# Performance work log

Measured on AMD Instinct MI355X. Metric: run time of the kernel, lower is better.

The kernel has to match this reference:

```python
import jax, jax.numpy as jnp
import numpy as np

D_MODEL = 1024
NUM_HEADS = 16
HEAD_DIM = D_MODEL // NUM_HEADS  # 64
# NOTE: the torch module passes scale=attention_head_size (NOT 1/sqrt(dh));
# we reproduce that exact math: scores are MULTIPLIED by head_dim.
SCALE = float(HEAD_DIM)

B, S = 2, 2048


def setup_inputs() -> dict:
    key = jax.random.key(0)
    ks = jax.random.split(key, 6)
    q = jax.random.normal(ks[0], (B, S, D_MODEL), dtype=jnp.float32)
    k = jax.random.normal(ks[1], (B, S, D_MODEL), dtype=jnp.float32)
    v = jax.random.normal(ks[2], (B, S, D_MODEL), dtype=jnp.float32)
    # Linear weights stored as [in, out]; scaled like typical init so the
    # (head_dim-scaled) logits stay numerically sane.
    w_std = 0.02
    Wq = jax.random.normal(ks[3], (D_MODEL, D_MODEL), dtype=jnp.float32) * w_std
    Wk = jax.random.normal(ks[4], (D_MODEL, D_MODEL), dtype=jnp.float32) * w_std
    Wv = jax.random.normal(ks[5], (D_MODEL, D_MODEL), dtype=jnp.float32) * w_std
    return {"q": q, "k": k, "v": v, "Wq": Wq, "Wk": Wk, "Wv": Wv}


def reference(q, k, v, Wq, Wk, Wv):
    Bq, Sq, _ = q.shape
    # QKV projections (qkv_bias=False), split into heads: [B, S, H, dh]
    qh = (q @ Wq).reshape(Bq, Sq, NUM_HEADS, HEAD_DIM)
    kh = (k @ Wk).reshape(Bq, Sq, NUM_HEADS, HEAD_DIM)
    vh = (v @ Wv).reshape(Bq, Sq, NUM_HEADS, HEAD_DIM)
    # Full materialized scores [B, H, Sq, Sk] -- the naive MHA pattern.
    sims = jnp.einsum("bqhd,bkhd->bhqk", qh, kh) * SCALE
    attn = jax.nn.softmax(sims, axis=-1)
    # Second matmul, then merge heads back: [B, S, D]
    out = jnp.einsum("bhqk,bkhd->bqhd", attn, vh).reshape(Bq, Sq, D_MODEL)
    return out
```

## Files before the change

### kernel.cpp

```cpp
#include <hip/hip_runtime.h>
#include <cstdint>
#include <cstddef>

typedef unsigned short u16;
typedef __bf16 bf16x8 __attribute__((ext_vector_type(8)));
typedef float f32x4 __attribute__((ext_vector_type(4)));
typedef unsigned int u32x4 __attribute__((ext_vector_type(4)));
typedef u16 u16x4 __attribute__((ext_vector_type(4)));

typedef __attribute__((address_space(3))) void lds_void;
typedef __attribute__((address_space(1))) void glb_void;

constexpr size_t XSZ = 4096ull * 1024ull;
constexpr size_t WSZ = 1024ull * 1024ull;
constexpr size_t OFF_XQH = 0;
constexpr size_t OFF_XQL = OFF_XQH + XSZ;
constexpr size_t OFF_XKH = OFF_XQL + XSZ;
constexpr size_t OFF_XKL = OFF_XKH + XSZ;
constexpr size_t OFF_XVH = OFF_XKL + XSZ;
constexpr size_t OFF_XVL = OFF_XVH + XSZ;
constexpr size_t OFF_WQH = OFF_XVL + XSZ;
constexpr size_t OFF_WQL = OFF_WQH + WSZ;
constexpr size_t OFF_WKH = OFF_WQL + WSZ;
constexpr size_t OFF_WKL = OFF_WKH + WSZ;
constexpr size_t OFF_WVH = OFF_WKL + WSZ;
constexpr size_t OFF_WVL = OFF_WVH + WSZ;
constexpr size_t OFF_QH  = OFF_WVL + WSZ;
constexpr size_t OFF_QL  = OFF_QH + XSZ;
constexpr size_t OFF_KH  = OFF_QL + XSZ;
constexpr size_t OFF_KL  = OFF_KH + XSZ;
constexpr size_t OFF_VH  = OFF_KL + XSZ;
constexpr size_t OFF_VT  = OFF_VH + XSZ;

__device__ __forceinline__ u16 f2b(float f) {
  unsigned u = __builtin_bit_cast(unsigned, f);
  return (u16)((u + 0x7FFFu + ((u >> 16) & 1u)) >> 16);
}
__device__ __forceinline__ float b2f(u16 h) {
  return __builtin_bit_cast(float, ((unsigned)h) << 16);
}
__device__ __forceinline__ bf16x8 ld8(const u16* p) {
  return __builtin_bit_cast(bf16x8, *(const u32x4*)p);
}
__device__ __forceinline__ unsigned pk2(float a, float b) {
#if __has_builtin(__builtin_amdgcn_cvt_pk_bf16_f32)
  auto v = __builtin_amdgcn_cvt_pk_bf16_f32(a, b);
  return __builtin_bit_cast(unsigned, v);
#else
  return (unsigned)f2b(a) | ((unsigned)f2b(b) << 16);
#endif
}
__device__ __forceinline__ void glds16(const u16* g, u16* l) {
  __builtin_amdgcn_global_load_lds((const glb_void*)g, (lds_void*)l, 16, 0, 0);
}
__device__ __forceinline__ int swz32(int row, int cg) {
  return row * 32 + ((cg ^ ((row >> 1) & 3)) * 8);
}
__device__ __forceinline__ int swz64(int row, int cg) {
  return row * 64 + ((cg ^ (row & 7)) * 8);
}

__global__ __launch_bounds__(256) void convert_x3(const float* __restrict__ q,
                                                  const float* __restrict__ k,
                                                  const float* __restrict__ v,
                                                  u16* __restrict__ ws) {
  int z = blockIdx.y;
  const float* in = (z == 0) ? q : (z == 1) ? k : v;
  u16* hi = ws + ((z == 0) ? OFF_XQH : (z == 1) ? OFF_XKH : OFF_XVH);
  u16* lo = ws + ((z == 0) ? OFF_XQL : (z == 1) ? OFF_XKL : OFF_XVL);
  size_t i = ((size_t)blockIdx.x * 256u + threadIdx.x) * 4u;
  float4 vv = *(const float4*)(in + i);
  float a[4] = {vv.x, vv.y, vv.z, vv.w};
  u16x4 hv, lv;
#pragma unroll
  for (int j = 0; j < 4; ++j) {
    u16 hb = f2b(a[j]);
    hv[j] = hb;
    lv[j] = f2b(a[j] - b2f(hb));
  }
  *(u16x4*)(hi + i) = hv;
  *(u16x4*)(lo + i) = lv;
}

__global__ __launch_bounds__(256) void convert_w3(const float* __restrict__ Wq,
                                                  const float* __restrict__ Wk,
                                                  const float* __restrict__ Wv,
                                                  u16* __restrict__ ws) {
  int z = blockIdx.z;
  const float* W = (z == 0) ? Wq : (z == 1) ? Wk : Wv;
  u16* hiT = ws + ((z == 0) ? OFF_WQH : (z == 1) ? OFF_WKH : OFF_WVH);
  u16* loT = ws + ((z == 0) ? OFF_WQL : (z == 1) ? OFF_WKL : OFF_WVL);
  __shared__ float tile[32][33];
  int n0 = blockIdx.x * 32, k0 = blockIdx.y * 32;
  int t = threadIdx.x;
  int r = t >> 3, c0 = (t & 7) * 4;
  float4 v = *(const float4*)(W + (size_t)(k0 + r) * 1024 + n0 + c0);
  tile[r][c0] = v.x; tile[r][c0 + 1] = v.y; tile[r][c0 + 2] = v.z; tile[r][c0 + 3] = v.w;
  __syncthreads();
  u16x4 hv, lv;
#pragma unroll
  for (int j = 0; j < 4; ++j) {
    float x = tile[c0 + j][r];
    u16 hb = f2b(x);
    hv[j] = hb;
    lv[j] = f2b(x - b2f(hb));
  }
  size_t o = (size_t)(n0 + r) * 1024 + k0 + c0;
  *(u16x4*)(hiT + o) = hv;
  *(u16x4*)(loT + o) = lv;
}

__global__ __launch_bounds__(256) void gemm_qkv(u16* __restrict__ ws) {
  __shared__ u16 lah[128 * 32];
  __shared__ u16 lal[128 * 32];
  __shared__ u16 lbh[128 * 32];
  __shared__ u16 lbl[128 * 32];
  int z = blockIdx.z;
  const u16 *Ah, *Al, *Bh, *Bl; u16 *Oh, *Ol; bool split;
  if (z == 0)      { Ah = ws + OFF_XQH; Al = ws + OFF_XQL; Bh = ws + OFF_WQH; Bl = ws + OFF_WQL; Oh = ws + OFF_QH; Ol = ws + OFF_QL; split = true; }
  else if (z == 1) { Ah = ws + OFF_XKH; Al = ws + OFF_XKL; Bh = ws + OFF_WKH; Bl = ws + OFF_WKL; Oh = ws + OFF_KH; Ol = ws + OFF_KL; split = true; }
  else             { Ah = ws + OFF_XVH; Al = ws + OFF_XVH; Bh = ws + OFF_WVH; Bl = ws + OFF_WVH; Oh = ws + OFF_VH; Ol = nullptr;    split = false; }
  int m0 = blockIdx.y * 128, n0 = blockIdx.x * 128;
  int t = threadIdx.x, lane = t & 63, wave = t >> 6;
  int wm = (wave >> 1) * 64, wn = (wave & 1) * 64;
  int rl = lane >> 2, cgl = lane & 3;
  f32x4 acc[4][4] = {};
  for (int kb = 0; kb < 32; ++kb) {
    int k0 = kb * 32;
    __syncthreads();
#pragma unroll
    for (int i = 0; i < 2; ++i) {
      int row = wave * 32 + i * 16 + rl;
      int cgg = cgl ^ ((row >> 1) & 3);
      size_t ga = (size_t)(m0 + row) * 1024 + k0 + cgg * 8;
      size_t gb = (size_t)(n0 + row) * 1024 + k0 + cgg * 8;
      int lbase = (wave * 32 + i * 16) * 32;
      glds16(Ah + ga, &lah[lbase]);
      glds16(Bh + gb, &lbh[lbase]);
      if (split) {
        glds16(Al + ga, &lal[lbase]);
        glds16(Bl + gb, &lbl[lbase]);
      }
    }
    __syncthreads();
    int cg0 = lane >> 4;
    bf16x8 afh[4], afl[4], bfh[4], bfl[4];
#pragma unroll
    for (int i = 0; i < 4; ++i) {
      int ra = wm + i * 16 + (lane & 15);
      int rb = wn + i * 16 + (lane & 15);
      afh[i] = ld8(&lah[swz32(ra, cg0)]);
      bfh[i] = ld8(&lbh[swz32(rb, cg0)]);
      if (split) {
        afl[i] = ld8(&lal[swz32(ra, cg0)]);
        bfl[i] = ld8(&lbl[swz32(rb, cg0)]);
      }
    }
#pragma unroll
    for (int mt = 0; mt < 4; ++mt)
#pragma unroll
      for (int nt = 0; nt < 4; ++nt) {
        acc[mt][nt] = __builtin_amdgcn_mfma_f32_16x16x32_bf16(afh[mt], bfh[nt], acc[mt][nt], 0, 0, 0);
        if (split) {
          acc[mt][nt] = __builtin_amdgcn_mfma_f32_16x16x32_bf16(afl[mt], bfh[nt], acc[mt][nt], 0, 0, 0);
          acc[mt][nt] = __builtin_amdgcn_mfma_f32_16x16x32_bf16(afh[mt], bfl[nt], acc[mt][nt], 0, 0, 0);
        }
      }
  }
#pragma unroll
  for (int mt = 0; mt < 4; ++mt)
#pragma unroll
    for (int nt = 0; nt < 4; ++nt)
#pragma unroll
      for (int r = 0; r < 4; ++r) {
        int gm = m0 + wm + mt * 16 + (lane >> 4) * 4 + r;
        int gn = n0 + wn + nt * 16 + (lane & 15);
        int bb = gm >> 11, s = gm & 2047, hh = gn >> 6, d = gn & 63;
        size_t oi = ((size_t)(bb * 16 + hh) * 2048 + s) * 64 + d;
        float val = acc[mt][nt][r];
        u16 hb = f2b(val);
        Oh[oi] = hb;
        if (Ol) Ol[oi] = f2b(val - b2f(hb));
      }
}

__global__ __launch_bounds__(256) void transpose_v(const u16* __restrict__ vh,
                                                   u16* __restrict__ vt) {
  __shared__ u16 tile[64][72];
  int bh = blockIdx.y;
  int s0 = blockIdx.x * 64;
  int t = threadIdx.x;
  for (int c = t; c < 512; c += 256) {
    int row = c >> 3, off = (c & 7) * 8;
    *(u32x4*)(&tile[row][off]) = *(const u32x4*)(vh + ((size_t)bh * 2048 + s0 + row) * 64 + off);
  }
  __syncthreads();
  int d = t >> 2, i0 = (t & 3) * 16;
  u16 vals[16];
#pragma unroll
  for (int i = 0; i < 16; ++i) vals[i] = tile[i0 + i][d];
  u16* outp = vt + ((size_t)bh * 64 + d) * 2048 + s0 + i0;
  *(u32x4*)(outp)     = *(u32x4*)(&vals[0]);
  *(u32x4*)(outp + 8) = *(u32x4*)(&vals[8]);
}

__global__ __launch_bounds__(256) void attn(const u16* __restrict__ ws,
                                            float* __restrict__ out) {
  constexpr int LD = 72;
  constexpr float CEXP = 92.33248261689366f;
  __shared__ u16 lkh[64 * 64];
  __shared__ u16 lkl[64 * 64];
  __shared__ u16 lvt[64 * 64];
  __shared__ u16 lp[4][16 * LD];
  const u16* Qh = ws + OFF_QH; const u16* Ql = ws + OFF_QL;
  const u16* Kh = ws + OFF_KH; const u16* Kl = ws + OFF_KL;
  const u16* Vt = ws + OFF_VT;
  int b = blockIdx.z, h = blockIdx.y;
  int q0 = blockIdx.x * 64;
  int t = threadIdx.x, lane = t & 63, wave = t >> 6;
  size_t hb = (size_t)(b * 16 + h) * (2048 * 64);
  bf16x8 onesf;
#pragma unroll
  for (int j = 0; j < 8; ++j) onesf[j] = __builtin_bit_cast(__bf16, (u16)0x3F80);
  int qrow = q0 + wave * 16 + (lane & 15);
  bf16x8 qfh[2], qfl[2];
#pragma unroll
  for (int ks = 0; ks < 2; ++ks) {
    size_t qo = hb + (size_t)qrow * 64 + ks * 32 + (lane >> 4) * 8;
    qfh[ks] = ld8(Qh + qo);
    qfl[ks] = ld8(Ql + qo);
  }
  float mi[4];
  f32x4 lsum = {};
  f32x4 o[4] = {};
#pragma unroll
  for (int r = 0; r < 4; ++r) mi[r] = -1e30f;
  int rl = lane >> 3, cgl = lane & 7;

  for (int kt = 0; kt < 32; ++kt) {
    __syncthreads();
#pragma unroll
    for (int i = 0; i < 2; ++i) {
      int row = wave * 16 + i * 8 + rl;
      int cgg = cgl ^ (row & 7);
      int lbase = (wave * 16 + i * 8) * 64;
      size_t gk = hb + (size_t)(kt * 64 + row) * 64 + cgg * 8;
      glds16(Kh + gk, &lkh[lbase]);
      glds16(Kl + gk, &lkl[lbase]);
      size_t gv = hb + (size_t)row * 2048 + kt * 64 + cgg * 8;
      glds16(Vt + gv, &lvt[lbase]);
    }
    __syncthreads();
    f32x4 sc[4] = {};
#pragma unroll
    for (int nt = 0; nt < 4; ++nt) {
#pragma unroll
      for (int ks = 0; ks < 2; ++ks) {
        int so = swz64(nt * 16 + (lane & 15), ks * 4 + (lane >> 4));
        bf16x8 bh_ = ld8(&lkh[so]);
        bf16x8 bl_ = ld8(&lkl[so]);
        sc[nt] = __builtin_amdgcn_mfma_f32_16x16x32_bf16(qfh[ks], bh_, sc[nt], 0, 0, 0);
        sc[nt] = __builtin_amdgcn_mfma_f32_16x16x32_bf16(qfl[ks], bh_, sc[nt], 0, 0, 0);
        sc[nt] = __builtin_amdgcn_mfma_f32_16x16x32_bf16(qfh[ks], bl_, sc[nt], 0, 0, 0);
      }
    }
    float mloc[4];
#pragma unroll
    for (int r = 0; r < 4; ++r)
      mloc[r] = fmaxf(fmaxf(sc[0][r], sc[1][r]), fmaxf(sc[2][r], sc[3][r]));
#pragma unroll
    for (int off = 1; off < 16; off <<= 1)
#pragma unroll
      for (int r = 0; r < 4; ++r)
        mloc[r] = fmaxf(mloc[r], __shfl_xor(mloc[r], off));
    float alpha[4], negmc[4];
#pragma unroll
    for (int r = 0; r < 4; ++r) {
      float mn = fmaxf(mi[r], mloc[r]);
      alpha[r] = exp2f((mi[r] - mn) * CEXP);
      mi[r] = mn;
      negmc[r] = -mn * CEXP;
    }
    int q4r = (lane >> 4) * 4;
    u16* lpw = &lp[wave][0];
#pragma unroll
    for (int nt = 0; nt < 4; ++nt) {
      float e0 = exp2f(fmaf(sc[nt][0], CEXP, negmc[0]));
      float e1 = exp2f(fmaf(sc[nt][1], CEXP, negmc[1]));
      float e2 = exp2f(fmaf(sc[nt][2], CEXP, negmc[2]));
      float e3 = exp2f(fmaf(sc[nt][3], CEXP, negmc[3]));
      unsigned u01 = pk2(e0, e1), u23 = pk2(e2, e3);
      int col = nt * 16 + (lane & 15);
      lpw[(q4r + 0) * LD + col] = (u16)(u01 & 0xffffu);
      lpw[(q4r + 1) * LD + col] = (u16)(u01 >> 16);
      lpw[(q4r + 2) * LD + col] = (u16)(u23 & 0xffffu);
      lpw[(q4r + 3) * LD + col] = (u16)(u23 >> 16);
    }
#pragma unroll
    for (int r = 0; r < 4; ++r) {
      lsum[r] *= alpha[r];
      o[0][r] *= alpha[r]; o[1][r] *= alpha[r]; o[2][r] *= alpha[r]; o[3][r] *= alpha[r];
    }
    asm volatile("s_waitcnt lgkmcnt(0)" ::: "memory");
    bf16x8 pa[2];
#pragma unroll
    for (int ks = 0; ks < 2; ++ks)
      pa[ks] = ld8(&lpw[(lane & 15) * LD + ks * 32 + (lane >> 4) * 8]);
    lsum = __builtin_amdgcn_mfma_f32_16x16x32_bf16(pa[0], onesf, lsum, 0, 0, 0);
    lsum = __builtin_amdgcn_mfma_f32_16x16x32_bf16(pa[1], onesf, lsum, 0, 0, 0);
#pragma unroll
    for (int nt = 0; nt < 4; ++nt)
#pragma unroll
      for (int ks = 0; ks < 2; ++ks) {
        bf16x8 bv = ld8(&lvt[swz64(nt * 16 + (lane & 15), ks * 4 + (lane >> 4))]);
        o[nt] = __builtin_amdgcn_mfma_f32_16x16x32_bf16(pa[ks], bv, o[nt], 0, 0, 0);
      }
  }
  float inv[4];
#pragma unroll
  for (int r = 0; r < 4; ++r) inv[r] = 1.0f / lsum[r];
#pragma unroll
  for (int nt = 0; nt < 4; ++nt)
#pragma unroll
    for (int r = 0; r < 4; ++r) {
      int srow = q0 + wave * 16 + (lane >> 4) * 4 + r;
      int d = nt * 16 + (lane & 15);
      out[(size_t)(b * 2048 + srow) * 1024 + h * 64 + d] = o[nt][r] * inv[r];
    }
}

extern "C" void kernel_launch(void* const* d_in, const int* in_sizes, int n_in,
                              void* d_out, int out_size, void* d_ws, size_t ws_size,
                              hipStream_t stream) {
  const float* q  = (const float*)d_in[0];
  const float* k  = (const float*)d_in[1];
  const float* v  = (const float*)d_in[2];
  const float* Wq = (const float*)d_in[3];
  const float* Wk = (const float*)d_in[4];
  const float* Wv = (const float*)d_in[5];
  u16* ws = (u16*)d_ws;
  float* out = (float*)d_out;

  convert_x3<<<dim3(4096, 3), 256, 0, stream>>>(q, k, v, ws);
  convert_w3<<<dim3(32, 32, 3), 256, 0, stream>>>(Wq, Wk, Wv, ws);
  gemm_qkv<<<dim3(8, 32, 3), 256, 0, stream>>>(ws);
  transpose_v<<<dim3(32, 32), 256, 0, stream>>>(ws + OFF_VH, ws + OFF_VT);
  attn<<<dim3(32, 16, 2), 256, 0, stream>>>(ws, out);
}
```

Baseline: 309.2 us.

## Fold softmax scale into Q projection and transpose score MFMA for per-lane row max

Multiplies the Q projection output by the log2-scaled softmax constant inside the QKV GEMM epilogue, so the attention loop can call exp2 directly on scores without a per-element FMA. Swaps the MFMA operand order so each lane holds one query row's scores, reducing the row-max to two cross-lane shuffles and a single running max per lane, with alpha redistributed via shuffles. P tiles are written to LDS as 8-byte vector stores with an XOR swizzle instead of scalar 2-byte stores into a padded layout. Scaling Q before the bf16 hi/lo split changes rounding slightly.

```diff
diff --git a/kernel.cpp b/kernel.cpp
--- a/kernel.cpp
+++ b/kernel.cpp
@@ -6,10 +6,13 @@
 typedef __bf16 bf16x8 __attribute__((ext_vector_type(8)));
 typedef float f32x4 __attribute__((ext_vector_type(4)));
 typedef unsigned int u32x4 __attribute__((ext_vector_type(4)));
+typedef unsigned int u32x2 __attribute__((ext_vector_type(2)));
 typedef u16 u16x4 __attribute__((ext_vector_type(4)));
 
 typedef __attribute__((address_space(3))) void lds_void;
 typedef __attribute__((address_space(1))) void glb_void;
+
+constexpr float CEXP = 92.33248261689366f;
 
 constexpr size_t XSZ = 4096ull * 1024ull;
 constexpr size_t WSZ = 1024ull * 1024ull;
@@ -120,6 +123,7 @@
   if (z == 0)      { Ah = ws + OFF_XQH; Al = ws + OFF_XQL; Bh = ws + OFF_WQH; Bl = ws + OFF_WQL; Oh = ws + OFF_QH; Ol = ws + OFF_QL; split = true; }
   else if (z == 1) { Ah = ws + OFF_XKH; Al = ws + OFF_XKL; Bh = ws + OFF_WKH; Bl = ws + OFF_WKL; Oh = ws + OFF_KH; Ol = ws + OFF_KL; split = true; }
   else             { Ah = ws + OFF_XVH; Al = ws + OFF_XVH; Bh = ws + OFF_WVH; Bl = ws + OFF_WVH; Oh = ws + OFF_VH; Ol = nullptr;    split = false; }
+  float oscale = (z == 0) ? CEXP : 1.0f;
   int m0 = blockIdx.y * 128, n0 = blockIdx.x * 128;
   int t = threadIdx.x, lane = t & 63, wave = t >> 6;
   int wm = (wave >> 1) * 64, wn = (wave & 1) * 64;
@@ -177,7 +181,7 @@
         int gn = n0 + wn + nt * 16 + (lane & 15);
         int bb = gm >> 11, s = gm & 2047, hh = gn >> 6, d = gn & 63;
         size_t oi = ((size_t)(bb * 16 + hh) * 2048 + s) * 64 + d;
-        float val = acc[mt][nt][r];
+        float val = acc[mt][nt][r] * oscale;
         u16 hb = f2b(val);
         Oh[oi] = hb;
         if (Ol) Ol[oi] = f2b(val - b2f(hb));
@@ -206,35 +210,32 @@
 
 __global__ __launch_bounds__(256) void attn(const u16* __restrict__ ws,
                                             float* __restrict__ out) {
-  constexpr int LD = 72;
-  constexpr float CEXP = 92.33248261689366f;
   __shared__ u16 lkh[64 * 64];
   __shared__ u16 lkl[64 * 64];
   __shared__ u16 lvt[64 * 64];
-  __shared__ u16 lp[4][16 * LD];
+  __shared__ u16 lp[4][16 * 64];
   const u16* Qh = ws + OFF_QH; const u16* Ql = ws + OFF_QL;
   const u16* Kh = ws + OFF_KH; const u16* Kl = ws + OFF_KL;
   const u16* Vt = ws + OFF_VT;
   int b = blockIdx.z, h = blockIdx.y;
   int q0 = blockIdx.x * 64;
   int t = threadIdx.x, lane = t & 63, wave = t >> 6;
+  int quad = lane >> 4, l15 = lane & 15;
   size_t hb = (size_t)(b * 16 + h) * (2048 * 64);
   bf16x8 onesf;
 #pragma unroll
   for (int j = 0; j < 8; ++j) onesf[j] = __builtin_bit_cast(__bf16, (u16)0x3F80);
-  int qrow = q0 + wave * 16 + (lane & 15);
+  int qrow = q0 + wave * 16 + l15;
   bf16x8 qfh[2], qfl[2];
 #pragma unroll
   for (int ks = 0; ks < 2; ++ks) {
-    size_t qo = hb + (size_t)qrow * 64 + ks * 32 + (lane >> 4) * 8;
+    size_t qo = hb + (size_t)qrow * 64 + ks * 32 + quad * 8;
     qfh[ks] = ld8(Qh + qo);
     qfl[ks] = ld8(Ql + qo);
   }
-  float mi[4];
+  float mi = -1e30f;
   f32x4 lsum = {};
   f32x4 o[4] = {};
-#pragma unroll
-  for (int r = 0; r < 4; ++r) mi[r] = -1e30f;
   int rl = lane >> 3, cgl = lane & 7;
 
   for (int kt = 0; kt < 32; ++kt) {
@@ -256,63 +257,57 @@
     for (int nt = 0; nt < 4; ++nt) {
 #pragma unroll
       for (int ks = 0; ks < 2; ++ks) {
-        int so = swz64(nt * 16 + (lane & 15), ks * 4 + (lane >> 4));
-        bf16x8 bh_ = ld8(&lkh[so]);
-        bf16x8 bl_ = ld8(&lkl[so]);
-        sc[nt] = __builtin_amdgcn_mfma_f32_16x16x32_bf16(qfh[ks], bh_, sc[nt], 0, 0, 0);
-        sc[nt] = __builtin_amdgcn_mfma_f32_16x16x32_bf16(qfl[ks], bh_, sc[nt], 0, 0, 0);
-        sc[nt] = __builtin_amdgcn_mfma_f32_16x16x32_bf16(qfh[ks], bl_, sc[nt], 0, 0, 0);
-      }
-    }
-    float mloc[4];
-#pragma unroll
-    for (int r = 0; r < 4; ++r)
-      mloc[r] = fmaxf(fmaxf(sc[0][r], sc[1][r]), fmaxf(sc[2][r], sc[3][r]));
-#pragma unroll
-    for (int off = 1; off < 16; off <<= 1)
-#pragma unroll
-      for (int r = 0; r < 4; ++r)
-        mloc[r] = fmaxf(mloc[r], __shfl_xor(mloc[r], off));
-    float alpha[4], negmc[4];
+        int so = swz64(nt * 16 + l15, ks * 4 + quad);
+        bf16x8 kh_ = ld8(&lkh[so]);
+        bf16x8 kl_ = ld8(&lkl[so]);
+        sc[nt] = __builtin_amdgcn_mfma_f32_16x16x32_bf16(kh_, qfh[ks], sc[nt], 0, 0, 0);
+        sc[nt] = __builtin_amdgcn_mfma_f32_16x16x32_bf16(kl_, qfh[ks], sc[nt], 0, 0, 0);
+        sc[nt] = __builtin_amdgcn_mfma_f32_16x16x32_bf16(kh_, qfl[ks], sc[nt], 0, 0, 0);
+      }
+    }
+    float mx = fmaxf(fmaxf(fmaxf(sc[0][0], sc[0][1]), fmaxf(sc[0][2], sc[0][3])),
+                     fmaxf(fmaxf(sc[1][0], sc[1][1]), fmaxf(sc[1][2], sc[1][3])));
+    float mx2 = fmaxf(fmaxf(fmaxf(sc[2][0], sc[2][1]), fmaxf(sc[2][2], sc[2][3])),
+                      fmaxf(fmaxf(sc[3][0], sc[3][1]), fmaxf(sc[3][2], sc[3][3])));
+    mx = fmaxf(mx, mx2);
+    mx = fmaxf(mx, __shfl_xor(mx, 16));
+    mx = fmaxf(mx, __shfl_xor(mx, 32));
+    float mn = fmaxf(mi, mx);
+    float alpha_s = exp2f(mi - mn);
+    mi = mn;
+    u16* lpw = &lp[wave][0];
+    int r7 = l15 & 7;
+#pragma unroll
+    for (int nt = 0; nt < 4; ++nt) {
+      float e0 = exp2f(sc[nt][0] - mn);
+      float e1 = exp2f(sc[nt][1] - mn);
+      float e2 = exp2f(sc[nt][2] - mn);
+      float e3 = exp2f(sc[nt][3] - mn);
+      unsigned u01 = pk2(e0, e1), u23 = pk2(e2, e3);
+      int c = nt * 2 + (quad >> 1);
+      int off = l15 * 64 + ((c ^ r7) * 8) + (quad & 1) * 4;
+      *(u32x2*)(&lpw[off]) = u32x2{u01, u23};
+    }
+    float av[4];
+#pragma unroll
+    for (int r = 0; r < 4; ++r) av[r] = __shfl(alpha_s, quad * 4 + r);
 #pragma unroll
     for (int r = 0; r < 4; ++r) {
-      float mn = fmaxf(mi[r], mloc[r]);
-      alpha[r] = exp2f((mi[r] - mn) * CEXP);
-      mi[r] = mn;
-      negmc[r] = -mn * CEXP;
-    }
-    int q4r = (lane >> 4) * 4;
-    u16* lpw = &lp[wave][0];
-#pragma unroll
-    for (int nt = 0; nt < 4; ++nt) {
-      float e0 = exp2f(fmaf(sc[nt][0], CEXP, negmc[0]));
-      float e1 = exp2f(fmaf(sc[nt][1], CEXP, negmc[1]));
-      float e2 = exp2f(fmaf(sc[nt][2], CEXP, negmc[2]));
-      float e3 = exp2f(fmaf(sc[nt][3], CEXP, negmc[3]));
-      unsigned u01 = pk2(e0, e1), u23 = pk2(e2, e3);
-      int col = nt * 16 + (lane & 15);
-      lpw[(q4r + 0) * LD + col] = (u16)(u01 & 0xffffu);
-      lpw[(q4r + 1) * LD + col] = (u16)(u01 >> 16);
-      lpw[(q4r + 2) * LD + col] = (u16)(u23 & 0xffffu);
-      lpw[(q4r + 3) * LD + col] = (u16)(u23 >> 16);
-    }
-#pragma unroll
-    for (int r = 0; r < 4; ++r) {
-      lsum[r] *= alpha[r];
-      o[0][r] *= alpha[r]; o[1][r] *= alpha[r]; o[2][r] *= alpha[r]; o[3][r] *= alpha[r];
+      lsum[r] *= av[r];
+      o[0][r] *= av[r]; o[1][r] *= av[r]; o[2][r] *= av[r]; o[3][r] *= av[r];
     }
     asm volatile("s_waitcnt lgkmcnt(0)" ::: "memory");
     bf16x8 pa[2];
 #pragma unroll
     for (int ks = 0; ks < 2; ++ks)
-      pa[ks] = ld8(&lpw[(lane & 15) * LD + ks * 32 + (lane >> 4) * 8]);
+      pa[ks] = ld8(&lpw[swz64(l15, ks * 4 + quad)]);
     lsum = __builtin_amdgcn_mfma_f32_16x16x32_bf16(pa[0], onesf, lsum, 0, 0, 0);
     lsum = __builtin_amdgcn_mfma_f32_16x16x32_bf16(pa[1], onesf, lsum, 0, 0, 0);
 #pragma unroll
     for (int nt = 0; nt < 4; ++nt)
 #pragma unroll
       for (int ks = 0; ks < 2; ++ks) {
-        bf16x8 bv = ld8(&lvt[swz64(nt * 16 + (lane & 15), ks * 4 + (lane >> 4))]);
+        bf16x8 bv = ld8(&lvt[swz64(nt * 16 + l15, ks * 4 + quad)]);
         o[nt] = __builtin_amdgcn_mfma_f32_16x16x32_bf16(pa[ks], bv, o[nt], 0, 0, 0);
       }
   }
@@ -323,8 +318,8 @@
   for (int nt = 0; nt < 4; ++nt)
 #pragma unroll
     for (int r = 0; r < 4; ++r) {
-      int srow = q0 + wave * 16 + (lane >> 4) * 4 + r;
-      int d = nt * 16 + (lane & 15);
+      int srow = q0 + wave * 16 + quad * 4 + r;
+      int d = nt * 16 + l15;
       out[(size_t)(b * 2048 + srow) * 1024 + h * 64 + d] = o[nt][r] * inv[r];
     }
 }
```

Result: faster. 296.6 us (-4.1%).
